# Performance work log

Measured on AMD Instinct MI355X. Metric: run time of the kernel, lower is better.

The kernel has to match this reference:

```python
import jax, jax.numpy as jnp
import numpy as np

# Rates 40MHz -> 60MHz => Fraction(1.5).limit_denominator(1000) = 3/2
UP, DOWN = 3, 2
MAX_RATE = max(UP, DOWN)
HALF_LEN = 10 * MAX_RATE                      # 30 (scipy.resample_poly default)
N_PRE_PAD = DOWN - (HALF_LEN % DOWN)          # 2
N_PRE_REMOVE = (HALF_LEN + N_PRE_PAD) // DOWN # 16
NUMTAPS_LS = 51
TAIL_ZEROS = 100
B, N = 8, 1048576


def _firwin_kaiser(numtaps, cutoff, beta):
    # scipy.signal.firwin(numtaps, cutoff, window=('kaiser', beta)), cutoff in Nyquist units
    m = np.arange(numtaps) - (numtaps - 1) / 2.0
    h = cutoff * np.sinc(cutoff * m)
    h *= np.kaiser(numtaps, beta)
    return h / h.sum()  # unit DC gain


def _band_int(k, f1, f2):
    # integral_{f1}^{f2} cos(pi*k*f) df, elementwise over integer array k
    k = np.asarray(k, dtype=float)
    safe = np.where(k == 0.0, 1.0, np.pi * k)
    return np.where(k == 0.0, f2 - f1, (np.sin(np.pi * k * f2) - np.sin(np.pi * k * f1)) / safe)


def _firls(numtaps, bands, desired):
    # Type-I linear-phase least-squares FIR (constant desired per band, unit weights)
    M = (numtaps - 1) // 2
    k = np.arange(M + 1)
    Q = np.zeros((M + 1, M + 1))
    rhs = np.zeros(M + 1)
    for f1, f2, d in zip(bands[0::2], bands[1::2], desired[0::2]):
        km = k[:, None] - k[None, :]
        kp = k[:, None] + k[None, :]
        Q += 0.5 * (_band_int(km, f1, f2) + _band_int(kp, f1, f2))
        rhs += d * _band_int(k, f1, f2)
    a = np.linalg.solve(Q, rhs)  # A(f) = sum_n a[n] cos(pi n f)
    half = a / 2.0
    half[0] = a[0]
    return np.concatenate([half[:0:-1], half])  # symmetric impulse response


def setup_inputs() -> dict:
    key = jax.random.key(0)
    x = jax.random.normal(key, (B, N), dtype=jnp.float32)
    # resample_poly anti-imaging filter, scaled by UP, with scipy's zero pre-padding
    h = _firwin_kaiser(2 * HALF_LEN + 1, 1.0 / MAX_RATE, 5.0) * UP
    h = np.concatenate([np.zeros(N_PRE_PAD), h])
    cutoff = DOWN / UP
    b = _firls(NUMTAPS_LS, [0.0, cutoff, cutoff + 0.1, 1.0], [1.0, 1.0, 0.0, 0.0])
    return {
        'x': x,
        'h_resample': jnp.asarray(h, jnp.float32),
        'b_fir': jnp.asarray(b, jnp.float32),
    }


def reference(x, h_resample, b_fir):
    b_sz, n = x.shape
    n_in = b_sz * n
    n_out = n_in * UP // DOWN + (1 if (n_in * UP) % DOWN else 0)
    xf = x.reshape(-1)
    Lh = h_resample.shape[0]
    # Fused polyphase resample: full convolution of UP-zero-stuffed signal
    # with h (flipped for true convolution), decimated by DOWN.
    y = jax.lax.conv_general_dilated(
        xf[None, None, :], h_resample[::-1][None, None, :],
        window_strides=(DOWN,), padding=[(Lh - 1, Lh - 1)],
        lhs_dilation=(UP,),
        dimension_numbers=('NCH', 'OIH', 'NCH'))[0, 0]
    u = y[N_PRE_REMOVE:N_PRE_REMOVE + n_out]               # == scipy.resample_poly
    up_padded = jnp.concatenate([u, jnp.zeros((TAIL_ZEROS,), x.dtype)])
    Lb = b_fir.shape[0]
    # lfilter(b, 1, .) == causal FIR: left-pad Lb-1 zeros, same-length output
    filt = jax.lax.conv_general_dilated(
        up_padded[None, None, :], b_fir[::-1][None, None, :],
        window_strides=(1,), padding=[(Lb - 1, 0)],
        dimension_numbers=('NCH', 'OIH', 'NCH'))[0, 0]
    total = n_out + TAIL_ZEROS
    per_b = total // b_sz
    return filt[:b_sz * per_b].reshape(b_sz, per_b)
```

## Files before the change

### kernel.cpp

```cpp
#include <hip/hip_runtime.h>


#define TPB 256
#define RPT 12
#define OTILE (TPB * RPT)
#define XTILE2 2112
#define NTAPS 55
#define CPSTRIDE 56

__global__ void build_coeffs(const float* __restrict__ h,
                             const float* __restrict__ b,
                             float* __restrict__ cp) {
    __shared__ float h_s[63];
    __shared__ float b_s[51];
    const int tid = threadIdx.x;
    if (tid < 63) h_s[tid] = h[tid];
    if (tid < 51) b_s[tid] = b[tid];
    __syncthreads();
    for (int idx = tid; idx < 3 * CPSTRIDE; idx += blockDim.x) {
        const int p = idx / CPSTRIDE;
        const int k = idx - p * CPSTRIDE;
        float acc = 0.0f;
        if (k < NTAPS) {
            const int j = p + 3 * k;
            for (int m = 0; m <= 50; ++m) {
                const int hi = j - 2 * m;
                if (hi >= 0 && hi <= 62) acc += b_s[m] * h_s[hi];
            }
        }
        cp[idx] = acc;
    }
}

__global__ __launch_bounds__(128) void boundary_fix(
    const float* __restrict__ x, const float* __restrict__ h,
    const float* __restrict__ b, float* __restrict__ out,
    int n_in, int n_out, int out_size)
{
    __shared__ float h_s[63];
    __shared__ float b_s[51];
    __shared__ float x_s[64];
    __shared__ float u_s[50];

    const int tid = threadIdx.x;
    if (tid < 63) h_s[tid] = h[tid];
    if (tid < 51) b_s[tid] = b[tid];

    if (blockIdx.x == 0) {
        if (tid < 44) x_s[tid] = (tid < n_in) ? x[tid] : 0.0f;
        __syncthreads();
        if (tid < 50) {
            const int s  = 2 * tid + 32;
            const int p0 = s % 3;
            const int q  = s / 3;
            float u = 0.0f;
            #pragma unroll
            for (int i = 0; i <= 20; ++i) {
                const int xi = q - i;
                u += h_s[p0 + 3 * i] * ((xi >= 0) ? x_s[xi] : 0.0f);
            }
            u_s[tid] = u;
        }
        __syncthreads();
        if (tid < 50) {
            float acc = 0.0f;
            for (int t = 0; t <= tid; ++t) acc += b_s[tid - t] * u_s[t];
            out[tid] = acc;
        }
    } else {
        const int t0   = n_out - 50;
        const int qmin = (2 * t0 + 32) / 3;
        const int xb   = qmin - 20;
        if (tid < 64) {
            const int xi = xb + tid;
            x_s[tid] = (xi >= 0 && xi < n_in) ? x[xi] : 0.0f;
        }
        __syncthreads();
        if (tid < 50) {
            const int t  = t0 + tid;
            const int s  = 2 * t + 32;
            const int p0 = s % 3;
            const int q  = s / 3;
            const int base = q - xb;
            float u = 0.0f;
            #pragma unroll
            for (int i = 0; i <= 20; ++i)
                u += h_s[p0 + 3 * i] * x_s[base - i];
            u_s[tid] = u;
        }
        __syncthreads();
        const int n_tail = out_size - n_out;
        if (tid < n_tail) {
            float acc = 0.0f;
            for (int j = tid; j <= 49; ++j) acc += b_s[tid + 50 - j] * u_s[j];
            out[n_out + tid] = acc;
        }
    }
}

#define GRP12(g, A, B, C, D) {                                          \
    const float4 q2 = c2q[g];                                           \
    const float4 q1 = c1q[g];                                           \
    const float4 q0 = c0q[g];                                           \
                                                               \
    a0  += q2.x * C.z;  a1  += q1.x * C.w;  a2  += q0.x * B.x;          \
    a3  += q2.x * B.x;  a4  += q1.x * B.y;  a5  += q0.x * B.z;          \
    a6  += q2.x * B.z;  a7  += q1.x * B.w;  a8  += q0.x * A.x;          \
    a9  += q2.x * A.x;  a10 += q1.x * A.y;  a11 += q0.x * A.z;          \
                                                               \
    a0  += q2.y * C.y;  a1  += q1.y * C.z;  a2  += q0.y * C.w;          \
    a3  += q2.y * C.w;  a4  += q1.y * B.x;  a5  += q0.y * B.y;          \
    a6  += q2.y * B.y;  a7  += q1.y * B.z;  a8  += q0.y * B.w;          \
    a9  += q2.y * B.w;  a10 += q1.y * A.x;  a11 += q0.y * A.y;          \
                                                               \
    a0  += q2.z * C.x;  a1  += q1.z * C.y;  a2  += q0.z * C.z;          \
    a3  += q2.z * C.z;  a4  += q1.z * C.w;  a5  += q0.z * B.x;          \
    a6  += q2.z * B.x;  a7  += q1.z * B.y;  a8  += q0.z * B.z;          \
    a9  += q2.z * B.z;  a10 += q1.z * B.w;  a11 += q0.z * A.x;          \
                                                               \
    a0  += q2.w * D.w;  a1  += q1.w * C.x;  a2  += q0.w * C.y;          \
    a3  += q2.w * C.y;  a4  += q1.w * C.z;  a5  += q0.w * C.w;          \
    a6  += q2.w * C.w;  a7  += q1.w * B.x;  a8  += q0.w * B.y;          \
    a9  += q2.w * B.y;  a10 += q1.w * B.z;  a11 += q0.w * B.w; }

#define GRP12T(g, A, B, C) {                                            \
    const float4 q2 = c2q[g];                                           \
    const float4 q1 = c1q[g];                                           \
    const float4 q0 = c0q[g];                                           \
    a0  += q2.x * C.z;  a1  += q1.x * C.w;  a2  += q0.x * B.x;          \
    a3  += q2.x * B.x;  a4  += q1.x * B.y;  a5  += q0.x * B.z;          \
    a6  += q2.x * B.z;  a7  += q1.x * B.w;  a8  += q0.x * A.x;          \
    a9  += q2.x * A.x;  a10 += q1.x * A.y;  a11 += q0.x * A.z;          \
    a0  += q2.y * C.y;  a1  += q1.y * C.z;  a2  += q0.y * C.w;          \
    a3  += q2.y * C.w;  a4  += q1.y * B.x;  a5  += q0.y * B.y;          \
    a6  += q2.y * B.y;  a7  += q1.y * B.z;  a8  += q0.y * B.w;          \
    a9  += q2.y * B.w;  a10 += q1.y * A.x;  a11 += q0.y * A.y;          \
    a0  += q2.z * C.x;  a1  += q1.z * C.y;  a2  += q0.z * C.z;          \
    a3  += q2.z * C.z;  a4  += q1.z * C.w;  a5  += q0.z * B.x;          \
    a6  += q2.z * B.x;  a7  += q1.z * B.y;  a8  += q0.z * B.z;          \
    a9  += q2.z * B.z;  a10 += q1.z * B.w;  a11 += q0.z * A.x; }

#define CONV12(SRC) {                                                   \
    const float4 w15 = SRC[15]; const float4 w14 = SRC[14];             \
    const float4 w13 = SRC[13]; const float4 w12 = SRC[12];             \
    const float4 w11 = SRC[11]; const float4 w10 = SRC[10];             \
    const float4 w9  = SRC[9];  const float4 w8  = SRC[8];              \
    const float4 w7  = SRC[7];  const float4 w6  = SRC[6];              \
    const float4 w5  = SRC[5];  const float4 w4  = SRC[4];              \
    const float4 w3  = SRC[3];  const float4 w2  = SRC[2];              \
    const float4 w1  = SRC[1];  const float4 w0  = SRC[0];              \
    __builtin_amdgcn_sched_barrier(0);                                  \
    GRP12( 0, w15, w14, w13, w12);                                      \
    GRP12( 1, w14, w13, w12, w11);                                      \
    GRP12( 2, w13, w12, w11, w10);                                      \
    GRP12( 3, w12, w11, w10, w9);                                       \
    GRP12( 4, w11, w10, w9,  w8);                                       \
    GRP12( 5, w10, w9,  w8,  w7);                                       \
    GRP12( 6, w9,  w8,  w7,  w6);                                       \
    GRP12( 7, w8,  w7,  w6,  w5);                                       \
    GRP12( 8, w7,  w6,  w5,  w4);                                       \
    GRP12( 9, w6,  w5,  w4,  w3);                                       \
    GRP12(10, w5,  w4,  w3,  w2);                                       \
    GRP12(11, w4,  w3,  w2,  w1);                                       \
    GRP12(12, w3,  w2,  w1,  w0);                                       \
    GRP12T(13, w2, w1, w0); }

__global__ __launch_bounds__(TPB) void fused_fast(
    const float* __restrict__ x, const float* __restrict__ cp,
    float* __restrict__ out, int n_in, int n_out)
{
    __shared__ float x_s[XTILE2];

    const int tid = threadIdx.x;
    const int o0  = blockIdx.x * OTILE;
    const int Qb  = (2 * o0 + 30) / 3;
    const int n_tile0 = Qb - 54;

    const float4* c2q = (const float4*)(cp + 2 * CPSTRIDE);
    const float4* c1q = (const float4*)(cp + 1 * CPSTRIDE);
    const float4* c0q = (const float4*)(cp + 0 * CPSTRIDE);

    float a0 = 0.f, a1 = 0.f, a2 = 0.f, a3  = 0.f, a4  = 0.f, a5  = 0.f;
    float a6 = 0.f, a7 = 0.f, a8 = 0.f, a9  = 0.f, a10 = 0.f, a11 = 0.f;

    const bool interior = (n_tile0 >= 0) && (Qb + 2050 <= n_in);
    if (interior) {
        const float4* gx4 = (const float4*)(x + n_tile0 + 8 * tid);
        CONV12(gx4);
    } else {
        for (int i = tid; i < XTILE2; i += TPB) {
            const int n = n_tile0 + i;
            x_s[i] = (n >= 0 && n < n_in) ? x[n] : 0.0f;
        }
        __syncthreads();
        const float4* xs4 = (const float4*)(x_s) + 2 * tid;
        CONV12(xs4);
    }

    const int ob = o0 + RPT * tid;
    if (ob >= 50 && ob + 11 < n_out) {
        float4* o4 = (float4*)(out + ob);
        o4[0] = make_float4(a0, a1, a2,  a3);
        o4[1] = make_float4(a4, a5, a6,  a7);
        o4[2] = make_float4(a8, a9, a10, a11);
    } else {
        const float accs[RPT] = {a0, a1, a2, a3, a4, a5, a6, a7, a8, a9, a10, a11};
#pragma unroll
        for (int d = 0; d < RPT; ++d) {
            const int o = ob + d;
            if (o >= 50 && o < n_out) out[o] = accs[d];
        }
    }
}

extern "C" void kernel_launch(void* const* d_in, const int* in_sizes, int n_in_arrs,
                              void* d_out, int out_size, void* d_ws, size_t ws_size,
                              hipStream_t stream) {
    const float* x = (const float*)d_in[0];
    const float* h = (const float*)d_in[1];
    const float* b = (const float*)d_in[2];
    float* out = (float*)d_out;
    float* cp  = (float*)d_ws;

    const int n_in  = in_sizes[0];
    const int n_out = (int)((long long)n_in * 3 / 2);

    build_coeffs<<<1, 64, 0, stream>>>(h, b, cp);

    const int nblocks = (n_out + OTILE - 1) / OTILE;
    fused_fast<<<nblocks, TPB, 0, stream>>>(x, cp, out, n_in, n_out);
    boundary_fix<<<2, 128, 0, stream>>>(x, h, b, out, n_in, n_out, out_size);
}
```

Baseline: 119.2 us.

## Process four tiles per block with double-buffered register prefetch of inputs

Each block now handles four consecutive output tiles, and the global input window for the next tile is loaded into a second register set while the current tile is convolved. The aim is to hide global load latency inside each thread instead of relying on many short-lived blocks. In exchange the kernel needs about 128 registers for the two input windows, which lowers occupancy. It also launches a quarter as many blocks and adds edge-path syncs inside conditionals.

```diff
diff --git a/kernel.cpp b/kernel.cpp
--- a/kernel.cpp
+++ b/kernel.cpp
@@ -4,6 +4,7 @@
 #define TPB 256
 #define RPT 12
 #define OTILE (TPB * RPT)
+#define TPBLK 4
 #define XTILE2 2112
 #define NTAPS 55
 #define CPSTRIDE 56
@@ -140,6 +141,32 @@
     a6  += q2.z * B.x;  a7  += q1.z * B.y;  a8  += q0.z * B.z;          \
     a9  += q2.z * B.z;  a10 += q1.z * B.w;  a11 += q0.z * A.x; }
 
+#define DECLW(S)                                                        \
+    float4 S##15, S##14, S##13, S##12, S##11, S##10, S##9, S##8,        \
+           S##7,  S##6,  S##5,  S##4,  S##3,  S##2,  S##1,  S##0;
+
+#define LOADW(S, SRC) {                                                 \
+    S##15 = SRC[15]; S##14 = SRC[14]; S##13 = SRC[13]; S##12 = SRC[12]; \
+    S##11 = SRC[11]; S##10 = SRC[10]; S##9  = SRC[9];  S##8  = SRC[8];  \
+    S##7  = SRC[7];  S##6  = SRC[6];  S##5  = SRC[5];  S##4  = SRC[4];  \
+    S##3  = SRC[3];  S##2  = SRC[2];  S##1  = SRC[1];  S##0  = SRC[0]; }
+
+#define CONVW(S) {                                                      \
+    GRP12( 0, S##15, S##14, S##13, S##12);                              \
+    GRP12( 1, S##14, S##13, S##12, S##11);                              \
+    GRP12( 2, S##13, S##12, S##11, S##10);                              \
+    GRP12( 3, S##12, S##11, S##10, S##9);                               \
+    GRP12( 4, S##11, S##10, S##9,  S##8);                               \
+    GRP12( 5, S##10, S##9,  S##8,  S##7);                               \
+    GRP12( 6, S##9,  S##8,  S##7,  S##6);                               \
+    GRP12( 7, S##8,  S##7,  S##6,  S##5);                               \
+    GRP12( 8, S##7,  S##6,  S##5,  S##4);                               \
+    GRP12( 9, S##6,  S##5,  S##4,  S##3);                               \
+    GRP12(10, S##5,  S##4,  S##3,  S##2);                               \
+    GRP12(11, S##4,  S##3,  S##2,  S##1);                               \
+    GRP12(12, S##3,  S##2,  S##1,  S##0);                               \
+    GRP12T(13, S##2, S##1, S##0); }
+
 #define CONV12(SRC) {                                                   \
     const float4 w15 = SRC[15]; const float4 w14 = SRC[14];             \
     const float4 w13 = SRC[13]; const float4 w12 = SRC[12];             \
@@ -165,51 +192,111 @@
     GRP12(12, w3,  w2,  w1,  w0);                                       \
     GRP12T(13, w2, w1, w0); }
 
+#define EDGE_COMPUTE(NT0) {                                             \
+    __syncthreads();                                                    \
+    for (int i = tid; i < XTILE2; i += TPB) {                           \
+        const int n = (NT0) + i;                                        \
+        x_s[i] = (n >= 0 && n < n_in) ? x[n] : 0.0f;                    \
+    }                                                                   \
+    __syncthreads();                                                    \
+    const float4* xs4 = (const float4*)(x_s) + 2 * tid;                 \
+    CONV12(xs4); }
+
+#define ZERO_ACC() { a0=0.f;a1=0.f;a2=0.f;a3=0.f;a4=0.f;a5=0.f;        \
+                     a6=0.f;a7=0.f;a8=0.f;a9=0.f;a10=0.f;a11=0.f; }
+
+#define STORE12(OB) {                                                   \
+    const int ob_ = (OB);                                               \
+    if (ob_ >= 50 && ob_ + 11 < n_out) {                                \
+        float4* o4 = (float4*)(out + ob_);   \
+        o4[0] = make_float4(a0, a1, a2,  a3);                           \
+        o4[1] = make_float4(a4, a5, a6,  a7);                           \
+        o4[2] = make_float4(a8, a9, a10, a11);                          \
+    } else {                                                            \
+        const float accs[RPT] = {a0,a1,a2,a3,a4,a5,a6,a7,a8,a9,a10,a11};\
+        _Pragma("unroll")                                               \
+        for (int d = 0; d < RPT; ++d) {                                 \
+            const int o = ob_ + d;                                      \
+            if (o >= 50 && o < n_out) out[o] = accs[d];                 \
+        }                                                               \
+    } }
+
 __global__ __launch_bounds__(TPB) void fused_fast(
     const float* __restrict__ x, const float* __restrict__ cp,
-    float* __restrict__ out, int n_in, int n_out)
+    float* __restrict__ out, int n_in, int n_out, int ntiles)
 {
     __shared__ float x_s[XTILE2];
 
     const int tid = threadIdx.x;
-    const int o0  = blockIdx.x * OTILE;
-    const int Qb  = (2 * o0 + 30) / 3;
-    const int n_tile0 = Qb - 54;
 
     const float4* c2q = (const float4*)(cp + 2 * CPSTRIDE);
     const float4* c1q = (const float4*)(cp + 1 * CPSTRIDE);
     const float4* c0q = (const float4*)(cp + 0 * CPSTRIDE);
 
-    float a0 = 0.f, a1 = 0.f, a2 = 0.f, a3  = 0.f, a4  = 0.f, a5  = 0.f;
-    float a6 = 0.f, a7 = 0.f, a8 = 0.f, a9  = 0.f, a10 = 0.f, a11 = 0.f;
-
-    const bool interior = (n_tile0 >= 0) && (Qb + 2050 <= n_in);
-    if (interior) {
-        const float4* gx4 = (const float4*)(x + n_tile0 + 8 * tid);
-        CONV12(gx4);
-    } else {
-        for (int i = tid; i < XTILE2; i += TPB) {
-            const int n = n_tile0 + i;
-            x_s[i] = (n >= 0 && n < n_in) ? x[n] : 0.0f;
-        }
-        __syncthreads();
-        const float4* xs4 = (const float4*)(x_s) + 2 * tid;
-        CONV12(xs4);
-    }
-
-    const int ob = o0 + RPT * tid;
-    if (ob >= 50 && ob + 11 < n_out) {
-        float4* o4 = (float4*)(out + ob);
-        o4[0] = make_float4(a0, a1, a2,  a3);
-        o4[1] = make_float4(a4, a5, a6,  a7);
-        o4[2] = make_float4(a8, a9, a10, a11);
-    } else {
-        const float accs[RPT] = {a0, a1, a2, a3, a4, a5, a6, a7, a8, a9, a10, a11};
-#pragma unroll
-        for (int d = 0; d < RPT; ++d) {
-            const int o = ob + d;
-            if (o >= 50 && o < n_out) out[o] = accs[d];
-        }
+    const int bt_0 = blockIdx.x * TPBLK;
+    const int bt_1 = bt_0 + 1;
+    const int bt_2 = bt_0 + 2;
+    const int bt_3 = bt_0 + 3;
+
+    const int nt0_0 = 2048 * bt_0 - 44;
+    const int nt0_1 = 2048 * bt_1 - 44;
+    const int nt0_2 = 2048 * bt_2 - 44;
+    const int nt0_3 = 2048 * bt_3 - 44;
+
+    const bool v0 = bt_0 < ntiles;
+    const bool v1 = bt_1 < ntiles;
+    const bool v2 = bt_2 < ntiles;
+    const bool v3 = bt_3 < ntiles;
+
+    const bool i0 = v0 && (nt0_0 >= 0) && (2048 * bt_0 + 2060 <= n_in);
+    const bool i1 = v1 && (nt0_1 >= 0) && (2048 * bt_1 + 2060 <= n_in);
+    const bool i2 = v2 && (nt0_2 >= 0) && (2048 * bt_2 + 2060 <= n_in);
+    const bool i3 = v3 && (nt0_3 >= 0) && (2048 * bt_3 + 2060 <= n_in);
+
+    const float4* s0 = (const float4*)(x + nt0_0 + 8 * tid);
+    const float4* s1 = (const float4*)(x + nt0_1 + 8 * tid);
+    const float4* s2 = (const float4*)(x + nt0_2 + 8 * tid);
+    const float4* s3 = (const float4*)(x + nt0_3 + 8 * tid);
+
+    DECLW(wA)
+    DECLW(wB)
+    float a0, a1, a2, a3, a4, a5, a6, a7, a8, a9, a10, a11;
+
+    if (i0) LOADW(wA, s0);
+    __builtin_amdgcn_sched_barrier(0);
+
+    if (i1) LOADW(wB, s1);
+    __builtin_amdgcn_sched_barrier(0);
+    if (v0) {
+        ZERO_ACC();
+        if (i0) { CONVW(wA); }
+        else    { EDGE_COMPUTE(nt0_0); }
+        STORE12(bt_0 * OTILE + RPT * tid);
+    }
+
+    if (i2) LOADW(wA, s2);
+    __builtin_amdgcn_sched_barrier(0);
+    if (v1) {
+        ZERO_ACC();
+        if (i1) { CONVW(wB); }
+        else    { EDGE_COMPUTE(nt0_1); }
+        STORE12(bt_1 * OTILE + RPT * tid);
+    }
+
+    if (i3) LOADW(wB, s3);
+    __builtin_amdgcn_sched_barrier(0);
+    if (v2) {
+        ZERO_ACC();
+        if (i2) { CONVW(wA); }
+        else    { EDGE_COMPUTE(nt0_2); }
+        STORE12(bt_2 * OTILE + RPT * tid);
+    }
+
+    if (v3) {
+        ZERO_ACC();
+        if (i3) { CONVW(wB); }
+        else    { EDGE_COMPUTE(nt0_3); }
+        STORE12(bt_3 * OTILE + RPT * tid);
     }
 }
 
@@ -227,7 +314,8 @@
 
     build_coeffs<<<1, 64, 0, stream>>>(h, b, cp);
 
-    const int nblocks = (n_out + OTILE - 1) / OTILE;
-    fused_fast<<<nblocks, TPB, 0, stream>>>(x, cp, out, n_in, n_out);
+    const int ntiles  = (n_out + OTILE - 1) / OTILE;
+    const int nblocks = (ntiles + TPBLK - 1) / TPBLK;
+    fused_fast<<<nblocks, TPB, 0, stream>>>(x, cp, out, n_in, n_out, ntiles);
     boundary_fix<<<2, 128, 0, stream>>>(x, h, b, out, n_in, n_out, out_size);
 }
```

Result: slower. 123.4 us (+3.5%).

## Stage input tile in swizzled LDS for all blocks with rolling register window

Applied to the files above, without the earlier changes.

Interior blocks now load the input tile once, coalesced into shared memory using an XOR swizzle, instead of each thread reading 16 overlapping float4s straight from global memory. The convolution then reads from LDS through a rotating six-register window rather than holding all sixteen float4s at once. This is meant to cut redundant global loads and register pressure, which may help occupancy. In exchange it adds a block-wide barrier and LDS traffic to every block.

```diff
diff --git a/kernel.cpp b/kernel.cpp
--- a/kernel.cpp
+++ b/kernel.cpp
@@ -4,9 +4,11 @@
 #define TPB 256
 #define RPT 12
 #define OTILE (TPB * RPT)
-#define XTILE2 2112
+#define NCHUNK 528
 #define NTAPS 55
 #define CPSTRIDE 56
+
+#define SLOT(c) ((c) ^ (((c) >> 3) & 7))
 
 __global__ void build_coeffs(const float* __restrict__ h,
                              const float* __restrict__ b,
@@ -140,62 +142,65 @@
     a6  += q2.z * B.x;  a7  += q1.z * B.y;  a8  += q0.z * B.z;          \
     a9  += q2.z * B.z;  a10 += q1.z * B.w;  a11 += q0.z * A.x; }
 
-#define CONV12(SRC) {                                                   \
-    const float4 w15 = SRC[15]; const float4 w14 = SRC[14];             \
-    const float4 w13 = SRC[13]; const float4 w12 = SRC[12];             \
-    const float4 w11 = SRC[11]; const float4 w10 = SRC[10];             \
-    const float4 w9  = SRC[9];  const float4 w8  = SRC[8];              \
-    const float4 w7  = SRC[7];  const float4 w6  = SRC[6];              \
-    const float4 w5  = SRC[5];  const float4 w4  = SRC[4];              \
-    const float4 w3  = SRC[3];  const float4 w2  = SRC[2];              \
-    const float4 w1  = SRC[1];  const float4 w0  = SRC[0];              \
-    __builtin_amdgcn_sched_barrier(0);                                  \
-    GRP12( 0, w15, w14, w13, w12);                                      \
-    GRP12( 1, w14, w13, w12, w11);                                      \
-    GRP12( 2, w13, w12, w11, w10);                                      \
-    GRP12( 3, w12, w11, w10, w9);                                       \
-    GRP12( 4, w11, w10, w9,  w8);                                       \
-    GRP12( 5, w10, w9,  w8,  w7);                                       \
-    GRP12( 6, w9,  w8,  w7,  w6);                                       \
-    GRP12( 7, w8,  w7,  w6,  w5);                                       \
-    GRP12( 8, w7,  w6,  w5,  w4);                                       \
-    GRP12( 9, w6,  w5,  w4,  w3);                                       \
-    GRP12(10, w5,  w4,  w3,  w2);                                       \
-    GRP12(11, w4,  w3,  w2,  w1);                                       \
-    GRP12(12, w3,  w2,  w1,  w0);                                       \
-    GRP12T(13, w2, w1, w0); }
-
 __global__ __launch_bounds__(TPB) void fused_fast(
     const float* __restrict__ x, const float* __restrict__ cp,
     float* __restrict__ out, int n_in, int n_out)
 {
-    __shared__ float x_s[XTILE2];
+    __shared__ float4 xs4[NCHUNK];
 
     const int tid = threadIdx.x;
-    const int o0  = blockIdx.x * OTILE;
-    const int Qb  = (2 * o0 + 30) / 3;
-    const int n_tile0 = Qb - 54;
+    const int bt  = blockIdx.x;
+    const int o0  = bt * OTILE;
+    const int n_tile0 = 2048 * bt - 44;
 
     const float4* c2q = (const float4*)(cp + 2 * CPSTRIDE);
     const float4* c1q = (const float4*)(cp + 1 * CPSTRIDE);
     const float4* c0q = (const float4*)(cp + 0 * CPSTRIDE);
 
+    const bool interior = (n_tile0 >= 0) && (n_tile0 + 4 * NCHUNK <= n_in);
+    if (interior) {
+        const float4* gx = (const float4*)(x + n_tile0);
+        const float4 g0 = gx[tid];
+        const float4 g1 = gx[tid + 256];
+        xs4[SLOT(tid)]       = g0;
+        xs4[SLOT(tid + 256)] = g1;
+        if (tid < NCHUNK - 512) {
+            xs4[SLOT(tid + 512)] = gx[tid + 512];
+        }
+    } else {
+        float* xsf = (float*)xs4;
+        for (int i = tid; i < 4 * NCHUNK; i += TPB) {
+            const int n = n_tile0 + i;
+            const float v = (n >= 0 && n < n_in) ? x[n] : 0.0f;
+            xsf[(SLOT(i >> 2) << 2) | (i & 3)] = v;
+        }
+    }
+    __syncthreads();
+
     float a0 = 0.f, a1 = 0.f, a2 = 0.f, a3  = 0.f, a4  = 0.f, a5  = 0.f;
     float a6 = 0.f, a7 = 0.f, a8 = 0.f, a9  = 0.f, a10 = 0.f, a11 = 0.f;
 
-    const bool interior = (n_tile0 >= 0) && (Qb + 2050 <= n_in);
-    if (interior) {
-        const float4* gx4 = (const float4*)(x + n_tile0 + 8 * tid);
-        CONV12(gx4);
-    } else {
-        for (int i = tid; i < XTILE2; i += TPB) {
-            const int n = n_tile0 + i;
-            x_s[i] = (n >= 0 && n < n_in) ? x[n] : 0.0f;
-        }
-        __syncthreads();
-        const float4* xs4 = (const float4*)(x_s) + 2 * tid;
-        CONV12(xs4);
-    }
+    const int cbase = 2 * tid;
+#define XS(j) xs4[SLOT(cbase + (j))]
+    {
+        float4 r0 = XS(15), r1 = XS(14), r2 = XS(13),
+               r3 = XS(12), r4 = XS(11), r5 = XS(10);
+        GRP12( 0, r0, r1, r2, r3);  r0 = XS(9);
+        GRP12( 1, r1, r2, r3, r4);  r1 = XS(8);
+        GRP12( 2, r2, r3, r4, r5);  r2 = XS(7);
+        GRP12( 3, r3, r4, r5, r0);  r3 = XS(6);
+        GRP12( 4, r4, r5, r0, r1);  r4 = XS(5);
+        GRP12( 5, r5, r0, r1, r2);  r5 = XS(4);
+        GRP12( 6, r0, r1, r2, r3);  r0 = XS(3);
+        GRP12( 7, r1, r2, r3, r4);  r1 = XS(2);
+        GRP12( 8, r2, r3, r4, r5);  r2 = XS(1);
+        GRP12( 9, r3, r4, r5, r0);  r3 = XS(0);
+        GRP12(10, r4, r5, r0, r1);
+        GRP12(11, r5, r0, r1, r2);
+        GRP12(12, r0, r1, r2, r3);
+        GRP12T(13, r1, r2, r3);
+    }
+#undef XS
 
     const int ob = o0 + RPT * tid;
     if (ob >= 50 && ob + 11 < n_out) {
```

Measured after the change: 117.0 us. Within noise of the previous version (-1.9%).
